# Optimization experiments

Hardware: AMD Instinct MI355X
Metric: run time of the kernel (lower is better)

The kernel has to match this reference:

```python
import jax, jax.numpy as jnp
import numpy as np

DEPTH, DIM, HEADS = 12, 768, 12
B, N = 2, 2048
HEAD_DIM = DIM // HEADS


def setup_inputs() -> dict:
    key = jax.random.key(0)
    ks = jax.random.split(key, 8)
    s = 0.02
    return {
        "x": jax.random.normal(ks[0], (B, N, DIM), jnp.float32),
        "sequence_ids": jnp.sort(jax.random.randint(ks[1], (B, N), 0, 8), axis=-1),
        "sequence_mask": jnp.zeros((B, N), dtype=bool),
        "ln1_w": jnp.ones((DEPTH, DIM), jnp.float32),
        "ln1_b": jnp.zeros((DEPTH, DIM), jnp.float32),
        "qkv_w": jax.random.normal(ks[2], (DEPTH, DIM, 3 * DIM), jnp.float32) * s,
        "qkv_b": jnp.zeros((DEPTH, 3 * DIM), jnp.float32),
        "proj_w": jax.random.normal(ks[3], (DEPTH, DIM, DIM), jnp.float32) * s,
        "proj_b": jnp.zeros((DEPTH, DIM), jnp.float32),
        "ls1_g": jnp.full((DEPTH, DIM), 1e-5, jnp.float32),
        "ln2_w": jnp.ones((DEPTH, DIM), jnp.float32),
        "ln2_b": jnp.zeros((DEPTH, DIM), jnp.float32),
        "fc1_w": jax.random.normal(ks[4], (DEPTH, DIM, 4 * DIM), jnp.float32) * s,
        "fc1_b": jnp.zeros((DEPTH, 4 * DIM), jnp.float32),
        "fc2_w": jax.random.normal(ks[5], (DEPTH, 4 * DIM, DIM), jnp.float32) * s,
        "fc2_b": jnp.zeros((DEPTH, DIM), jnp.float32),
        "ls2_g": jnp.full((DEPTH, DIM), 1e-5, jnp.float32),
        "r": 0,
    }


def _layernorm(x, w, b, eps=1e-5):
    m = x.mean(-1, keepdims=True)
    v = ((x - m) ** 2).mean(-1, keepdims=True)
    return (x - m) * jax.lax.rsqrt(v + eps) * w + b


def _attention(x, attn_mask, qkv_w, qkv_b, proj_w, proj_b):
    b, n, c = x.shape
    qkv = (x @ qkv_w + qkv_b).reshape(b, n, 3, HEADS, HEAD_DIM)
    qkv = jnp.transpose(qkv, (2, 0, 3, 1, 4))  # [3, B, H, N, hd]
    q, k, v = qkv[0], qkv[1], qkv[2]
    attn = jnp.einsum("bhqd,bhkd->bhqk", q, k) * (HEAD_DIM ** -0.5)
    neg_inf = jnp.finfo(attn.dtype).min
    attn = jnp.where(attn_mask[:, None, :, :], neg_inf, attn)  # broadcast over heads
    attn = jax.nn.softmax(attn, axis=-1)
    out = jnp.einsum("bhqk,bhkd->bhqd", attn, v)
    out = jnp.transpose(out, (0, 2, 1, 3)).reshape(b, n, c)
    return out @ proj_w + proj_b


def reference(x, sequence_ids, sequence_mask, ln1_w, ln1_b, qkv_w, qkv_b,
              proj_w, proj_b, ls1_g, ln2_w, ln2_b, fc1_w, fc1_b,
              fc2_w, fc2_b, ls2_g, r):
    # attn_mask: True where attention is NOT allowed
    attn_mask = sequence_ids[:, :, None] != sequence_ids[:, None, :]
    attn_mask = attn_mask | sequence_mask[:, :, None] | sequence_mask[:, None, :]
    for i in range(DEPTH):
        h = _layernorm(x, ln1_w[i], ln1_b[i])
        h = _attention(h, attn_mask, qkv_w[i], qkv_b[i], proj_w[i], proj_b[i])
        x = x + h * ls1_g[i]
        h = _layernorm(x, ln2_w[i], ln2_b[i])
        h = jax.nn.gelu(h @ fc1_w[i] + fc1_b[i], approximate=False) @ fc2_w[i] + fc2_b[i]
        x = x + h * ls2_g[i]
    return x
```

## Files before the change

kernel.cpp:

```cpp
#include <hip/hip_runtime.h>

#define NDEPTH 12
#define NDIM 768
#define NHEADS 12
#define NB 2
#define NSEQ 2048
#define MTOK (NB*NSEQ)

typedef short bf16x8 __attribute__((ext_vector_type(8)));
typedef float f32x4 __attribute__((ext_vector_type(4)));
typedef unsigned short u16;
typedef unsigned int u32;

#define L2E 1.44269504088896f

__device__ inline u16 f2bf(float f){
  union { float f; u32 u; } x; x.f = f;
  u32 r = x.u + 0x7fffu + ((x.u >> 16) & 1u);
  return (u16)(r >> 16);
}

__device__ inline f32x4 mfma16(bf16x8 a, bf16x8 b, f32x4 c){
  return __builtin_amdgcn_mfma_f32_16x16x32_bf16(a, b, c, 0, 0, 0);
}

#define GLOAD_LDS(gsrc, ldst) __builtin_amdgcn_global_load_lds( \
    (const __attribute__((address_space(1))) u32*)(gsrc), \
    (__attribute__((address_space(3))) u32*)(ldst), 16, 0, 0)

__global__ __launch_bounds__(256) void ln_kernel(const float* __restrict__ x,
    const float* __restrict__ w, const float* __restrict__ b,
    u16* __restrict__ out){
  int wv = threadIdx.x >> 6, lane = threadIdx.x & 63;
  int row = blockIdx.x * 4 + wv;
  const float* xr = x + (size_t)row * NDIM;
  float v[12];
  #pragma unroll
  for (int j = 0; j < 12; j++) v[j] = xr[lane + 64*j];
  float s = 0.f;
  #pragma unroll
  for (int j = 0; j < 12; j++) s += v[j];
  #pragma unroll
  for (int m = 1; m < 64; m <<= 1) s += __shfl_xor(s, m);
  float mean = s * (1.0f/768.0f);
  float q = 0.f;
  #pragma unroll
  for (int j = 0; j < 12; j++){ float d = v[j]-mean; q += d*d; }
  #pragma unroll
  for (int m = 1; m < 64; m <<= 1) q += __shfl_xor(q, m);
  float rs = rsqrtf(q * (1.0f/768.0f) + 1e-5f);
  u16* orow = out + (size_t)row * NDIM;
  #pragma unroll
  for (int j = 0; j < 12; j++){
    int c = lane + 64*j;
    orow[c] = f2bf((v[j]-mean)*rs*w[c] + b[c]);
  }
}

__device__ inline void wtrans_body(const float* __restrict__ in,
    u16* __restrict__ out, int K, int N, int n0, int k0, float* tile){
  int t = threadIdx.x;
  #pragma unroll
  for (int j = 0; j < 16; j++){
    int idx = t + j*256;
    int r = idx >> 6, c = idx & 63;
    tile[r*65 + c] = in[(size_t)(k0+r)*N + n0 + c];
  }
  __syncthreads();
  #pragma unroll
  for (int j = 0; j < 16; j++){
    int idx = t + j*256;
    int c = idx >> 6, r = idx & 63;
    out[(size_t)(n0+c)*K + k0 + r] = f2bf(tile[r*65 + c]);
  }
}

__global__ __launch_bounds__(256) void wtrans_kernel(const float* __restrict__ in,
    u16* __restrict__ out, int K, int N){
  __shared__ float tile[64*65];
  wtrans_body(in, out, K, N, blockIdx.x*64, blockIdx.y*64, tile);
}

__global__ __launch_bounds__(256) void wtrans4_kernel(
    const float* __restrict__ qkvw, const float* __restrict__ projw,
    const float* __restrict__ fc1w, const float* __restrict__ fc2w,
    u16* __restrict__ wq, u16* __restrict__ wp,
    u16* __restrict__ w1, u16* __restrict__ w2){
  __shared__ float tile[64*65];
  int bid = blockIdx.x;
  const float* in; u16* out; int K, N, tl;
  if (bid < 432){        in = qkvw; out = wq; K = 768;  N = 2304; tl = bid; }
  else if (bid < 576){   in = projw; out = wp; K = 768; N = 768;  tl = bid - 432; }
  else if (bid < 1152){  in = fc1w; out = w1; K = 768;  N = 3072; tl = bid - 576; }
  else {                 in = fc2w; out = w2; K = 3072; N = 768;  tl = bid - 1152; }
  int ntn = N >> 6;
  int n0 = (tl % ntn) << 6, k0 = (tl / ntn) << 6;
  wtrans_body(in, out, K, N, n0, k0, tile);
}

template<int BN, int EPI>
__global__ __launch_bounds__(256) void gemm_kernel(
    const u16* __restrict__ A, const u16* __restrict__ Wt,
    const float* __restrict__ bias, const float* __restrict__ g,
    u16* __restrict__ outb, float* __restrict__ xres,
    int M, int N, int K)
{
  constexpr int WN = BN/2;
  constexpr int NFR = WN/16;
  __shared__ u16 As[2][128*64];
  __shared__ u16 Bs[2][BN*64];
  int nwg = gridDim.x;
  int bid = (blockIdx.x & 7) * (nwg >> 3) + (blockIdx.x >> 3);
  int nt = N / BN;
  int bm = bid / nt, bn = bid % nt;
  int m0 = bm*128, n0 = bn*BN;
  int t = threadIdx.x, lane = t & 63, wv = t >> 6;
  int wm = (wv >> 1) * 64, wn = (wv & 1) * WN;
  f32x4 acc[4][NFR] = {};
  int fr = lane & 15, fg = lane >> 4;

  auto stage = [&](int bf, int k0){
    #pragma unroll
    for (int i = 0; i < 4; i++){
      int off = t*16 + i*4096;
      int row = off >> 7, cb = off & 127;
      const char* src = (const char*)A + ((size_t)(m0+row)*K + k0)*2 + (cb ^ ((row&7)<<4));
      GLOAD_LDS(src, (char*)As[bf] + off);
    }
    #pragma unroll
    for (int i = 0; i < BN/32; i++){
      int off = t*16 + i*4096;
      int row = off >> 7, cb = off & 127;
      const char* src = (const char*)Wt + ((size_t)(n0+row)*K + k0)*2 + (cb ^ ((row&7)<<4));
      GLOAD_LDS(src, (char*)Bs[bf] + off);
    }
  };

  stage(0, 0);
  int cur = 0;
  for (int k0 = 0; k0 < K; k0 += 64){
    __syncthreads();
    if (k0 + 64 < K) stage(cur ^ 1, k0 + 64);

    bf16x8 af[4][2], bfv[NFR][2];
    #pragma unroll
    for (int mi = 0; mi < 4; mi++)
      #pragma unroll
      for (int kh = 0; kh < 2; kh++){
        int row = wm + mi*16 + fr;
        int off = (row*128 + kh*64 + fg*16) ^ ((row&7)<<4);
        af[mi][kh] = *(const bf16x8*)((const char*)As[cur] + off);
      }
    #pragma unroll
    for (int ni = 0; ni < NFR; ni++)
      #pragma unroll
      for (int kh = 0; kh < 2; kh++){
        int row = wn + ni*16 + fr;
        int off = (row*128 + kh*64 + fg*16) ^ ((row&7)<<4);
        bfv[ni][kh] = *(const bf16x8*)((const char*)Bs[cur] + off);
      }
    #pragma unroll
    for (int mi = 0; mi < 4; mi++)
      #pragma unroll
      for (int ni = 0; ni < NFR; ni++){
        acc[mi][ni] = mfma16(af[mi][0], bfv[ni][0], acc[mi][ni]);
        acc[mi][ni] = mfma16(af[mi][1], bfv[ni][1], acc[mi][ni]);
      }
    cur ^= 1;
  }

  int fq = fg << 2;
  #pragma unroll
  for (int mi = 0; mi < 4; mi++){
    #pragma unroll
    for (int ni = 0; ni < NFR; ni++){
      int col = n0 + wn + ni*16 + fr;
      float bv = bias[col];
      #pragma unroll
      for (int r = 0; r < 4; r++){
        int row = m0 + wm + mi*16 + fq + r;
        float v = acc[mi][ni][r] + bv;
        if (EPI == 0){
          outb[(size_t)row * N + col] = f2bf(v);
        } else if (EPI == 1){
          float ge = 0.5f * v * (1.0f + erff(v * 0.70710678118f));
          outb[(size_t)row * N + col] = f2bf(ge);
        } else {
          xres[(size_t)row * N + col] += v * g[col];
        }
      }
    }
  }
}

__global__ __launch_bounds__(256) void attn_kernel(
    const u16* __restrict__ qkv, const int* __restrict__ sid,
    const unsigned char* __restrict__ smask, u16* __restrict__ outb)
{
  __shared__ u16 Ks[64][72];
  __shared__ u16 Vs[64][72];
  __shared__ u16 Ps[4][16][72];
  int nwg = gridDim.x;
  int blk = (blockIdx.x & 7) * (nwg >> 3) + (blockIdx.x >> 3);
  int qt = blk & 31; int bh = blk >> 5;
  int b = bh / NHEADS, h = bh % NHEADS;
  int t = threadIdx.x, lane = t & 63, wv = t >> 6;
  int q0 = qt << 6;
  size_t rowbase = (size_t)b * NSEQ;
  int fr = lane & 15, fg8 = (lane >> 4) << 3, fq = (lane >> 4) << 2;

  int qrow = q0 + (wv << 4) + fr;
  const u16* qp = qkv + (rowbase + qrow) * 2304 + h*64 + fg8;
  bf16x8 qf0 = *(const bf16x8*)qp;
  bf16x8 qf1 = *(const bf16x8*)(qp + 32);

  int qlo = sid[rowbase + q0];
  int qhi = sid[rowbase + q0 + 63];

  int sq[4]; int mq[4];
  #pragma unroll
  for (int r = 0; r < 4; r++){
    int qr = q0 + (wv << 4) + fq + r;
    sq[r] = sid[rowbase + qr];
    mq[r] = smask[rowbase + qr];
  }
  float m[4], l[4]; f32x4 o[4] = {};
  #pragma unroll
  for (int r = 0; r < 4; r++){ m[r] = -3.0e38f; l[r] = 0.f; }

  int skk = t >> 2, sd = (t & 3) << 4;

  for (int kt = 0; kt < NSEQ/64; kt++){
    int klo = sid[rowbase + (kt << 6)];
    int khi = sid[rowbase + (kt << 6) + 63];
    if (khi < qlo || klo > qhi) continue;

    __syncthreads();
    int krow = (kt << 6) + skk;
    const u16* kp = qkv + (rowbase + krow) * 2304 + 768 + h*64 + sd;
    *(uint4*)&Ks[skk][sd]     = *(const uint4*)kp;
    *(uint4*)&Ks[skk][sd + 8] = *(const uint4*)(kp + 8);
    const u16* vp = kp + 768;
    uint4 v0 = *(const uint4*)vp, v1 = *(const uint4*)(vp + 8);
    {
      const u16* vv = (const u16*)&v0;
      #pragma unroll
      for (int i = 0; i < 8; i++) Vs[sd + i][skk] = vv[i];
      vv = (const u16*)&v1;
      #pragma unroll
      for (int i = 0; i < 8; i++) Vs[sd + 8 + i][skk] = vv[i];
    }
    int ks[4]; int mk[4];
    #pragma unroll
    for (int s2 = 0; s2 < 4; s2++){
      int kk = (kt << 6) + (s2 << 4) + fr;
      ks[s2] = sid[rowbase + kk];
      mk[s2] = smask[rowbase + kk];
    }
    __syncthreads();

    f32x4 S[4];
    #pragma unroll
    for (int s2 = 0; s2 < 4; s2++){
      bf16x8 kf0 = *(const bf16x8*)&Ks[(s2 << 4) + fr][fg8];
      bf16x8 kf1 = *(const bf16x8*)&Ks[(s2 << 4) + fr][fg8 + 32];
      f32x4 s = {};
      s = mfma16(qf0, kf0, s);
      s = mfma16(qf1, kf1, s);
      #pragma unroll
      for (int r = 0; r < 4; r++){
        float v = s[r] * 0.125f;
        bool msk = (mq[r] | mk[s2]) || (sq[r] != ks[s2]);
        S[s2][r] = msk ? -3.0e38f : v;
      }
    }
    float mn[4], sf[4], rs[4];
    #pragma unroll
    for (int r = 0; r < 4; r++){
      float mx = fmaxf(fmaxf(S[0][r], S[1][r]), fmaxf(S[2][r], S[3][r]));
      #pragma unroll
      for (int d = 1; d < 16; d <<= 1) mx = fmaxf(mx, __shfl_xor(mx, d));
      mn[r] = fmaxf(m[r], mx);
      sf[r] = exp2f((m[r] - mn[r]) * L2E);
      rs[r] = 0.f;
    }
    #pragma unroll
    for (int s2 = 0; s2 < 4; s2++){
      #pragma unroll
      for (int r = 0; r < 4; r++){
        float p = exp2f((S[s2][r] - mn[r]) * L2E);
        rs[r] += p;
        Ps[wv][fq + r][(s2 << 4) + fr] = f2bf(p);
      }
    }
    #pragma unroll
    for (int r = 0; r < 4; r++){
      #pragma unroll
      for (int d = 1; d < 16; d <<= 1) rs[r] += __shfl_xor(rs[r], d);
      l[r] = l[r] * sf[r] + rs[r];
      m[r] = mn[r];
    }
    #pragma unroll
    for (int dsub = 0; dsub < 4; dsub++)
      #pragma unroll
      for (int r = 0; r < 4; r++) o[dsub][r] *= sf[r];
    __syncthreads();
    #pragma unroll
    for (int kg = 0; kg < 2; kg++){
      bf16x8 pf = *(const bf16x8*)&Ps[wv][fr][(kg << 5) + fg8];
      #pragma unroll
      for (int dsub = 0; dsub < 4; dsub++){
        bf16x8 vf = *(const bf16x8*)&Vs[(dsub << 4) + fr][(kg << 5) + fg8];
        o[dsub] = mfma16(pf, vf, o[dsub]);
      }
    }
  }

  #pragma unroll
  for (int dsub = 0; dsub < 4; dsub++){
    #pragma unroll
    for (int r = 0; r < 4; r++){
      int row = q0 + (wv << 4) + fq + r;
      int col = h*64 + (dsub << 4) + fr;
      outb[(rowbase + row) * NDIM + col] = f2bf(o[dsub][r] / l[r]);
    }
  }
}

extern "C" void kernel_launch(void* const* d_in, const int* in_sizes, int n_in,
                              void* d_out, int out_size, void* d_ws, size_t ws_size,
                              hipStream_t stream) {
  const float* x_in = (const float*)d_in[0];
  const int* sid = (const int*)d_in[1];
  const unsigned char* smask = (const unsigned char*)d_in[2];
  const float* ln1w = (const float*)d_in[3];
  const float* ln1b = (const float*)d_in[4];
  const float* qkvw = (const float*)d_in[5];
  const float* qkvb = (const float*)d_in[6];
  const float* projw = (const float*)d_in[7];
  const float* projb = (const float*)d_in[8];
  const float* ls1 = (const float*)d_in[9];
  const float* ln2w = (const float*)d_in[10];
  const float* ln2b = (const float*)d_in[11];
  const float* fc1w = (const float*)d_in[12];
  const float* fc1b = (const float*)d_in[13];
  const float* fc2w = (const float*)d_in[14];
  const float* fc2b = (const float*)d_in[15];
  const float* ls2 = (const float*)d_in[16];

  float* x = (float*)d_out;
  char* ws = (char*)d_ws;
  u16* hbuf   = (u16*)ws;
  u16* qkvbuf = (u16*)(ws + (size_t)6291456);
  u16* abuf   = (u16*)(ws + (size_t)25165824);
  u16* mbuf   = (u16*)(ws + (size_t)31457280);
  const size_t WT0 = 56623104;

  bool fused_wt = ws_size >= (size_t)(WT0 + 14155776);
  u16* wq; u16* wp; u16* w1; u16* w2;
  if (fused_wt){
    wq = (u16*)(ws + WT0);
    wp = wq + (size_t)2304*768;
    w1 = wp + (size_t)768*768;
    w2 = w1 + (size_t)768*3072;
  } else {
    wq = wp = w1 = w2 = (u16*)(ws + WT0);
  }

  hipMemcpyAsync(x, x_in, (size_t)MTOK*NDIM*4, hipMemcpyDeviceToDevice, stream);

  for (int i = 0; i < NDEPTH; i++){
    const float* qw = qkvw + (size_t)i*NDIM*2304;
    const float* pw = projw + (size_t)i*NDIM*NDIM;
    const float* f1 = fc1w + (size_t)i*NDIM*3072;
    const float* f2 = fc2w + (size_t)i*3072*NDIM;

    if (fused_wt){
      wtrans4_kernel<<<1728, 256, 0, stream>>>(qw, pw, f1, f2, wq, wp, w1, w2);
    }
    ln_kernel<<<MTOK/4, 256, 0, stream>>>(x, ln1w + i*NDIM, ln1b + i*NDIM, hbuf);
    if (!fused_wt)
      wtrans_kernel<<<dim3(2304/64, 768/64), 256, 0, stream>>>(qw, wq, NDIM, 2304);
    gemm_kernel<128,0><<<(MTOK/128)*(2304/128), 256, 0, stream>>>(
        hbuf, wq, qkvb + (size_t)i*2304, nullptr, qkvbuf, nullptr, MTOK, 2304, NDIM);
    attn_kernel<<<NB*NHEADS*(NSEQ/64), 256, 0, stream>>>(qkvbuf, sid, smask, abuf);
    if (!fused_wt)
      wtrans_kernel<<<dim3(768/64, 768/64), 256, 0, stream>>>(pw, wp, NDIM, NDIM);
    gemm_kernel<64,2><<<(MTOK/128)*(NDIM/64), 256, 0, stream>>>(
        abuf, wp, projb + (size_t)i*NDIM, ls1 + (size_t)i*NDIM,
        nullptr, x, MTOK, NDIM, NDIM);
    ln_kernel<<<MTOK/4, 256, 0, stream>>>(x, ln2w + i*NDIM, ln2b + i*NDIM, hbuf);
    if (!fused_wt)
      wtrans_kernel<<<dim3(3072/64, 768/64), 256, 0, stream>>>(f1, w1, NDIM, 3072);
    gemm_kernel<128,1><<<(MTOK/128)*(3072/128), 256, 0, stream>>>(
        hbuf, w1, fc1b + (size_t)i*3072, nullptr, mbuf, nullptr, MTOK, 3072, NDIM);
    if (!fused_wt)
      wtrans_kernel<<<dim3(768/64, 3072/64), 256, 0, stream>>>(f2, w2, 3072, NDIM);
    gemm_kernel<64,2><<<(MTOK/128)*(NDIM/64), 256, 0, stream>>>(
        mbuf, w2, fc2b + (size_t)i*NDIM, ls2 + (size_t)i*NDIM,
        nullptr, x, MTOK, NDIM, 3072);
  }
}
```

Baseline: 2.340 ms.

## Use 8-wave GEMM tiles with BK=32 and fuse LN1 into weight-transpose launch

The GEMM kernel goes from 4 to 8 waves per block (512 threads). The K-step drops from 64 to 32, which halves LDS per buffer and changes the swizzle to match. Each wave now computes a smaller sub-tile, which aims to raise wave occupancy and latency hiding. Separately, the first layernorm is merged into the fused weight-transpose kernel to save one launch per layer. The trade-off is twice as many barriers per K, fewer MFMAs between syncs, and less register-level reuse per wave.

```diff
diff --git a/kernel.cpp b/kernel.cpp
--- a/kernel.cpp
+++ b/kernel.cpp
@@ -28,33 +28,39 @@
     (const __attribute__((address_space(1))) u32*)(gsrc), \
     (__attribute__((address_space(3))) u32*)(ldst), 16, 0, 0)
 
+__device__ inline void ln_body(const float* __restrict__ x,
+    const float* __restrict__ w, const float* __restrict__ b,
+    u16* __restrict__ out, int blk){
+  int wv = threadIdx.x >> 6, lane = threadIdx.x & 63;
+  int row = blk * 4 + wv;
+  const float* xr = x + (size_t)row * NDIM;
+  float v[12];
+  #pragma unroll
+  for (int j = 0; j < 12; j++) v[j] = xr[lane + 64*j];
+  float s = 0.f;
+  #pragma unroll
+  for (int j = 0; j < 12; j++) s += v[j];
+  #pragma unroll
+  for (int m = 1; m < 64; m <<= 1) s += __shfl_xor(s, m);
+  float mean = s * (1.0f/768.0f);
+  float q = 0.f;
+  #pragma unroll
+  for (int j = 0; j < 12; j++){ float d = v[j]-mean; q += d*d; }
+  #pragma unroll
+  for (int m = 1; m < 64; m <<= 1) q += __shfl_xor(q, m);
+  float rs = rsqrtf(q * (1.0f/768.0f) + 1e-5f);
+  u16* orow = out + (size_t)row * NDIM;
+  #pragma unroll
+  for (int j = 0; j < 12; j++){
+    int c = lane + 64*j;
+    orow[c] = f2bf((v[j]-mean)*rs*w[c] + b[c]);
+  }
+}
+
 __global__ __launch_bounds__(256) void ln_kernel(const float* __restrict__ x,
     const float* __restrict__ w, const float* __restrict__ b,
     u16* __restrict__ out){
-  int wv = threadIdx.x >> 6, lane = threadIdx.x & 63;
-  int row = blockIdx.x * 4 + wv;
-  const float* xr = x + (size_t)row * NDIM;
-  float v[12];
-  #pragma unroll
-  for (int j = 0; j < 12; j++) v[j] = xr[lane + 64*j];
-  float s = 0.f;
-  #pragma unroll
-  for (int j = 0; j < 12; j++) s += v[j];
-  #pragma unroll
-  for (int m = 1; m < 64; m <<= 1) s += __shfl_xor(s, m);
-  float mean = s * (1.0f/768.0f);
-  float q = 0.f;
-  #pragma unroll
-  for (int j = 0; j < 12; j++){ float d = v[j]-mean; q += d*d; }
-  #pragma unroll
-  for (int m = 1; m < 64; m <<= 1) q += __shfl_xor(q, m);
-  float rs = rsqrtf(q * (1.0f/768.0f) + 1e-5f);
-  u16* orow = out + (size_t)row * NDIM;
-  #pragma unroll
-  for (int j = 0; j < 12; j++){
-    int c = lane + 64*j;
-    orow[c] = f2bf((v[j]-mean)*rs*w[c] + b[c]);
-  }
+  ln_body(x, w, b, out, blockIdx.x);
 }
 
 __device__ inline void wtrans_body(const float* __restrict__ in,
@@ -81,13 +87,17 @@
   wtrans_body(in, out, K, N, blockIdx.x*64, blockIdx.y*64, tile);
 }
 
-__global__ __launch_bounds__(256) void wtrans4_kernel(
+__global__ __launch_bounds__(256) void lnwt_kernel(
+    const float* __restrict__ x, const float* __restrict__ lw,
+    const float* __restrict__ lb, u16* __restrict__ lout,
     const float* __restrict__ qkvw, const float* __restrict__ projw,
     const float* __restrict__ fc1w, const float* __restrict__ fc2w,
     u16* __restrict__ wq, u16* __restrict__ wp,
     u16* __restrict__ w1, u16* __restrict__ w2){
   __shared__ float tile[64*65];
   int bid = blockIdx.x;
+  if (bid < 1024){ ln_body(x, lw, lb, lout, bid); return; }
+  bid -= 1024;
   const float* in; u16* out; int K, N, tl;
   if (bid < 432){        in = qkvw; out = wq; K = 768;  N = 2304; tl = bid; }
   else if (bid < 576){   in = projw; out = wp; K = 768; N = 768;  tl = bid - 432; }
@@ -99,81 +109,77 @@
 }
 
 template<int BN, int EPI>
-__global__ __launch_bounds__(256) void gemm_kernel(
+__global__ __launch_bounds__(512) void gemm_kernel(
     const u16* __restrict__ A, const u16* __restrict__ Wt,
     const float* __restrict__ bias, const float* __restrict__ g,
     u16* __restrict__ outb, float* __restrict__ xres,
     int M, int N, int K)
 {
-  constexpr int WN = BN/2;
-  constexpr int NFR = WN/16;
-  __shared__ u16 As[2][128*64];
-  __shared__ u16 Bs[2][BN*64];
+  constexpr int WGM = (BN == 128) ? 2 : 4;
+  constexpr int WGN = 8 / WGM;
+  constexpr int WTM = 128 / WGM;
+  constexpr int WTN = BN / WGN;
+  constexpr int MI = WTM / 16;
+  constexpr int NI = WTN / 16;
+  __shared__ u16 As[2][128*32];
+  __shared__ u16 Bs[2][BN*32];
   int nwg = gridDim.x;
   int bid = (blockIdx.x & 7) * (nwg >> 3) + (blockIdx.x >> 3);
   int nt = N / BN;
   int bm = bid / nt, bn = bid % nt;
   int m0 = bm*128, n0 = bn*BN;
   int t = threadIdx.x, lane = t & 63, wv = t >> 6;
-  int wm = (wv >> 1) * 64, wn = (wv & 1) * WN;
-  f32x4 acc[4][NFR] = {};
+  int wm = (wv / WGN) * WTM, wn = (wv % WGN) * WTN;
+  f32x4 acc[MI][NI] = {};
   int fr = lane & 15, fg = lane >> 4;
 
   auto stage = [&](int bf, int k0){
-    #pragma unroll
-    for (int i = 0; i < 4; i++){
-      int off = t*16 + i*4096;
-      int row = off >> 7, cb = off & 127;
-      const char* src = (const char*)A + ((size_t)(m0+row)*K + k0)*2 + (cb ^ ((row&7)<<4));
+    {
+      int off = t*16;
+      int row = off >> 6, cb = off & 63;
+      const char* src = (const char*)A + ((size_t)(m0+row)*K + k0)*2 + (cb ^ ((row&3)<<4));
       GLOAD_LDS(src, (char*)As[bf] + off);
     }
-    #pragma unroll
-    for (int i = 0; i < BN/32; i++){
-      int off = t*16 + i*4096;
-      int row = off >> 7, cb = off & 127;
-      const char* src = (const char*)Wt + ((size_t)(n0+row)*K + k0)*2 + (cb ^ ((row&7)<<4));
+    if (BN == 128 || t < 256){
+      int off = t*16;
+      int row = off >> 6, cb = off & 63;
+      const char* src = (const char*)Wt + ((size_t)(n0+row)*K + k0)*2 + (cb ^ ((row&3)<<4));
       GLOAD_LDS(src, (char*)Bs[bf] + off);
     }
   };
 
   stage(0, 0);
   int cur = 0;
-  for (int k0 = 0; k0 < K; k0 += 64){
+  for (int k0 = 0; k0 < K; k0 += 32){
     __syncthreads();
-    if (k0 + 64 < K) stage(cur ^ 1, k0 + 64);
-
-    bf16x8 af[4][2], bfv[NFR][2];
-    #pragma unroll
-    for (int mi = 0; mi < 4; mi++)
-      #pragma unroll
-      for (int kh = 0; kh < 2; kh++){
-        int row = wm + mi*16 + fr;
-        int off = (row*128 + kh*64 + fg*16) ^ ((row&7)<<4);
-        af[mi][kh] = *(const bf16x8*)((const char*)As[cur] + off);
-      }
-    #pragma unroll
-    for (int ni = 0; ni < NFR; ni++)
-      #pragma unroll
-      for (int kh = 0; kh < 2; kh++){
-        int row = wn + ni*16 + fr;
-        int off = (row*128 + kh*64 + fg*16) ^ ((row&7)<<4);
-        bfv[ni][kh] = *(const bf16x8*)((const char*)Bs[cur] + off);
-      }
-    #pragma unroll
-    for (int mi = 0; mi < 4; mi++)
-      #pragma unroll
-      for (int ni = 0; ni < NFR; ni++){
-        acc[mi][ni] = mfma16(af[mi][0], bfv[ni][0], acc[mi][ni]);
-        acc[mi][ni] = mfma16(af[mi][1], bfv[ni][1], acc[mi][ni]);
-      }
+    if (k0 + 32 < K) stage(cur ^ 1, k0 + 32);
+
+    bf16x8 af[MI], bfv[NI];
+    #pragma unroll
+    for (int mi = 0; mi < MI; mi++){
+      int row = wm + mi*16 + fr;
+      int off = (row*64 + fg*16) ^ ((row&3)<<4);
+      af[mi] = *(const bf16x8*)((const char*)As[cur] + off);
+    }
+    #pragma unroll
+    for (int ni = 0; ni < NI; ni++){
+      int row = wn + ni*16 + fr;
+      int off = (row*64 + fg*16) ^ ((row&3)<<4);
+      bfv[ni] = *(const bf16x8*)((const char*)Bs[cur] + off);
+    }
+    #pragma unroll
+    for (int mi = 0; mi < MI; mi++)
+      #pragma unroll
+      for (int ni = 0; ni < NI; ni++)
+        acc[mi][ni] = mfma16(af[mi], bfv[ni], acc[mi][ni]);
     cur ^= 1;
   }
 
   int fq = fg << 2;
   #pragma unroll
-  for (int mi = 0; mi < 4; mi++){
-    #pragma unroll
-    for (int ni = 0; ni < NFR; ni++){
+  for (int mi = 0; mi < MI; mi++){
+    #pragma unroll
+    for (int ni = 0; ni < NI; ni++){
       int col = n0 + wn + ni*16 + fr;
       float bv = bias[col];
       #pragma unroll
@@ -376,27 +382,28 @@
     const float* f2 = fc2w + (size_t)i*3072*NDIM;
 
     if (fused_wt){
-      wtrans4_kernel<<<1728, 256, 0, stream>>>(qw, pw, f1, f2, wq, wp, w1, w2);
-    }
-    ln_kernel<<<MTOK/4, 256, 0, stream>>>(x, ln1w + i*NDIM, ln1b + i*NDIM, hbuf);
-    if (!fused_wt)
+      lnwt_kernel<<<2752, 256, 0, stream>>>(x, ln1w + i*NDIM, ln1b + i*NDIM, hbuf,
+                                            qw, pw, f1, f2, wq, wp, w1, w2);
+    } else {
+      ln_kernel<<<MTOK/4, 256, 0, stream>>>(x, ln1w + i*NDIM, ln1b + i*NDIM, hbuf);
       wtrans_kernel<<<dim3(2304/64, 768/64), 256, 0, stream>>>(qw, wq, NDIM, 2304);
-    gemm_kernel<128,0><<<(MTOK/128)*(2304/128), 256, 0, stream>>>(
+    }
+    gemm_kernel<128,0><<<(MTOK/128)*(2304/128), 512, 0, stream>>>(
         hbuf, wq, qkvb + (size_t)i*2304, nullptr, qkvbuf, nullptr, MTOK, 2304, NDIM);
     attn_kernel<<<NB*NHEADS*(NSEQ/64), 256, 0, stream>>>(qkvbuf, sid, smask, abuf);
     if (!fused_wt)
       wtrans_kernel<<<dim3(768/64, 768/64), 256, 0, stream>>>(pw, wp, NDIM, NDIM);
-    gemm_kernel<64,2><<<(MTOK/128)*(NDIM/64), 256, 0, stream>>>(
+    gemm_kernel<64,2><<<(MTOK/128)*(NDIM/64), 512, 0, stream>>>(
         abuf, wp, projb + (size_t)i*NDIM, ls1 + (size_t)i*NDIM,
         nullptr, x, MTOK, NDIM, NDIM);
     ln_kernel<<<MTOK/4, 256, 0, stream>>>(x, ln2w + i*NDIM, ln2b + i*NDIM, hbuf);
     if (!fused_wt)
       wtrans_kernel<<<dim3(3072/64, 768/64), 256, 0, stream>>>(f1, w1, NDIM, 3072);
-    gemm_kernel<128,1><<<(MTOK/128)*(3072/128), 256, 0, stream>>>(
+    gemm_kernel<128,1><<<(MTOK/128)*(3072/128), 512, 0, stream>>>(
         hbuf, w1, fc1b + (size_t)i*3072, nullptr, mbuf, nullptr, MTOK, 3072, NDIM);
     if (!fused_wt)
       wtrans_kernel<<<dim3(768/64, 3072/64), 256, 0, stream>>>(f2, w2, 3072, NDIM);
-    gemm_kernel<64,2><<<(MTOK/128)*(NDIM/64), 256, 0, stream>>>(
+    gemm_kernel<64,2><<<(MTOK/128)*(NDIM/64), 512, 0, stream>>>(
         mbuf, w2, fc2b + (size_t)i*NDIM, ls2 + (size_t)i*NDIM,
         nullptr, x, MTOK, NDIM, 3072);
   }
```

Result: faster. 2.202 ms (-5.9%).
